# Kernel optimization log

Measured on AMD Instinct MI355X. Metric: run time of the kernel, lower is better.

The kernel has to match this reference:

```python
import jax, jax.numpy as jnp
import numpy as np

N_ANGLES = 8


def setup_inputs() -> dict:
    key = jax.random.key(0)
    ks = jax.random.split(key, 6)
    N, in_size, out_size, K = 20000, 64, 64, 8
    M = N_ANGLES * N            # block-Laplacian dim = 160000
    E = M * 16                  # avg degree 16 -> 2.56M nnz
    x = jax.random.normal(ks[0], (N, in_size), dtype=jnp.float32)
    ls_vals = jax.random.normal(ks[1], (E,), dtype=jnp.float32) * 0.1
    ls_rows = jax.random.randint(ks[2], (E,), 0, M, dtype=jnp.int32)
    ls_cols = jax.random.randint(ks[3], (E,), 0, M, dtype=jnp.int32)
    weight = jax.random.normal(ks[4], (K, N_ANGLES * in_size, out_size), dtype=jnp.float32) * 0.05
    bias = jnp.zeros((out_size,), dtype=jnp.float32)
    return {"x": x, "ls_vals": ls_vals, "weight": weight, "bias": bias,
            "ls_rows": ls_rows, "ls_cols": ls_cols}


def reference(x, ls_vals, weight, bias, ls_rows, ls_cols):
    N, in_size = x.shape
    K = weight.shape[0]
    M = N_ANGLES * N

    def spmm(T):
        # sparse [M,M] @ dense [M,in] via gather + segment_sum
        return jax.ops.segment_sum(ls_vals[:, None] * T[ls_cols], ls_rows,
                                   num_segments=M)

    def feat(T):
        # [n_angles*N, in] -> [N, n_angles*in] (angle-major per node)
        return T.reshape(N_ANGLES, N, in_size).transpose(1, 0, 2).reshape(N, -1)

    Tx0 = jnp.tile(x, (N_ANGLES, 1))                  # [M, in]
    out = feat(Tx0) @ weight[0]                       # [N, out]
    Tx1 = spmm(Tx0)
    out = out + feat(Tx1) @ weight[1]
    for k in range(2, K):
        Tx2 = 2.0 * spmm(Tx1) - Tx0
        out = out + feat(Tx2) @ weight[k]
        Tx0, Tx1 = Tx1, Tx2
    return out + bias
```

## Files before the change

kernel.cpp:

```cpp
#include <hip/hip_runtime.h>
#include <hip/hip_bf16.h>

#define N_NODES 20000
#define NANG 8
#define CH 64
#define M_ROWS (NANG * N_NODES)
#define E_EDGES (M_ROWS * 16)
#define K_CHEB 8
#define WK_STRIDE (NANG * CH * CH)
#define BROWS 256
#define NB (M_ROWS / BROWS)
#define NCHUNK 320
#define CHUNK (E_EDGES / NCHUNK)
#define SPMM_BLOCKS (M_ROWS / 4)
#define KCAT 3648
#define SK_TOTAL 114
#define BCAP 5120
#define GROWS 32
#define GEMM_BLOCKS (N_NODES / GROWS)

typedef short short8 __attribute__((ext_vector_type(8)));
typedef float f32x4 __attribute__((ext_vector_type(4)));

__device__ __forceinline__ float bf2f(ushort u) {
    return __uint_as_float((unsigned int)u << 16);
}


__global__ __launch_bounds__(256) void count_kernel(const int* __restrict__ rows,
                                                    int* __restrict__ chunk_cnt) {
    __shared__ int h[NB];
    int c = blockIdx.x, tid = threadIdx.x;
    for (int i = tid; i < NB; i += 256) h[i] = 0;
    __syncthreads();
    int base = c * CHUNK;
    for (int i = tid; i < CHUNK; i += 256) atomicAdd(&h[rows[base + i] >> 8], 1);
    __syncthreads();
    for (int i = tid; i < NB; i += 256) chunk_cnt[(size_t)c * NB + i] = h[i];
}

__global__ __launch_bounds__(512) void bscan2_kernel(int* __restrict__ chunk_cnt,
                                                     int* __restrict__ btotal) {
    __shared__ int s[512];
    int b = blockIdx.x, t = threadIdx.x;
    int v = (t < NCHUNK) ? chunk_cnt[(size_t)t * NB + b] : 0;
    s[t] = v;
    __syncthreads();
    for (int off = 1; off < 512; off <<= 1) {
        int u = (t >= off) ? s[t - off] : 0;
        __syncthreads();
        s[t] += u;
        __syncthreads();
    }
    if (t < NCHUNK) chunk_cnt[(size_t)t * NB + b] = s[t] - v;
    if (t == 511) btotal[b] = s[511];
}

__global__ void bscan_kernel(const int* __restrict__ btotal, int* __restrict__ bstart) {
    __shared__ int s[1024];
    int t = threadIdx.x;
    int v = (t < NB) ? btotal[t] : 0;
    s[t] = v;
    __syncthreads();
    for (int off = 1; off < 1024; off <<= 1) {
        int u = (t >= off) ? s[t - off] : 0;
        __syncthreads();
        s[t] += u;
        __syncthreads();
    }
    if (t < NB) bstart[t] = s[t] - v;
    if (t == 1023) bstart[NB] = s[1023];
}

__global__ __launch_bounds__(256) void scatter_kernel(
        const int* __restrict__ rows, const int* __restrict__ cols,
        const float* __restrict__ vals, const int* __restrict__ chunk_cnt,
        const int* __restrict__ bstart, int2* __restrict__ bedges) {
    __shared__ int loff[NB];
    int c = blockIdx.x, tid = threadIdx.x;
    for (int i = tid; i < NB; i += 256)
        loff[i] = chunk_cnt[(size_t)c * NB + i] + bstart[i];
    __syncthreads();
    int base = c * CHUNK;
    for (int i = tid; i < CHUNK; i += 256) {
        int e = base + i;
        int r = rows[e];
        int p = atomicAdd(&loff[r >> 8], 1);
        bedges[p] = make_int2(cols[e] | ((r & 255) << 18), __float_as_int(vals[e]));
    }
}

__global__ __launch_bounds__(256) void bucket_group_kernel(
        const int* __restrict__ bstart, const int2* __restrict__ bin,
        int2* __restrict__ bout, int* __restrict__ row_start) {
    __shared__ int cnt[BROWS];
    __shared__ int pref[BROWS];
    __shared__ int fill[BROWS];
    __shared__ int2 ob[BCAP];
    int b = blockIdx.x, tid = threadIdx.x;
    int s = bstart[b], e = bstart[b + 1];
    int n = e - s;
    cnt[tid] = 0;
    __syncthreads();
    int2 eds[20];
    int ni = 0;
    for (int i = tid; i < n; i += 256, ++ni) {
        int2 ed = bin[s + i];
        if (ni < 20) eds[ni] = ed;
        atomicAdd(&cnt[(ed.x >> 18) & 255], 1);
    }
    __syncthreads();
    int v = cnt[tid];
    pref[tid] = v;
    __syncthreads();
#pragma unroll
    for (int off = 1; off < 256; off <<= 1) {
        int u = (tid >= off) ? pref[tid - off] : 0;
        __syncthreads();
        pref[tid] += u;
        __syncthreads();
    }
    int my_excl = pref[tid] - v;
    __syncthreads();
    pref[tid] = my_excl;
    fill[tid] = my_excl;
    __syncthreads();

    if (n <= BCAP) {
        ni = 0;
        for (int i = tid; i < n; i += 256, ++ni) {
            int2 ed = (ni < 20) ? eds[ni] : bin[s + i];
            int p = atomicAdd(&fill[(ed.x >> 18) & 255], 1);
            ob[p] = make_int2(ed.x & 0x3ffff, ed.y);
        }
        __syncthreads();
        for (int i = tid; i < n; i += 256)
            bout[s + i] = ob[i];
    } else {
        ni = 0;
        for (int i = tid; i < n; i += 256, ++ni) {
            int2 ed = (ni < 20) ? eds[ni] : bin[s + i];
            int p = atomicAdd(&fill[(ed.x >> 18) & 255], 1);
            bout[s + p] = make_int2(ed.x & 0x3ffff, ed.y);
        }
    }
    row_start[b * BROWS + tid] = s + pref[tid];
    if (b == NB - 1 && tid == 0) row_start[M_ROWS] = e;
}


__global__ void xconv_kernel(const float* __restrict__ x, ushort* __restrict__ xb) {
    int i = blockIdx.x * 256 + threadIdx.x;
    __hip_bfloat16 v = __float2bfloat16(x[i]);
    xb[i] = *(ushort*)&v;
}

__global__ void wcat_kernel(const float* __restrict__ W, ushort* __restrict__ Wcat) {
    int idx = blockIdx.x * 256 + threadIdx.x;
    int n   = idx / KCAT;
    int kkc = idx - n * KCAT;
    float v;
    if (kkc < 64) {
        v = 0.f;
#pragma unroll
        for (int a = 0; a < NANG; ++a) v += W[(a * 64 + kkc) * 64 + n];
    } else {
        int k  = ((kkc - 64) >> 9) + 1;
        int kk = (kkc - 64) & 511;
        v = W[(size_t)k * WK_STRIDE + kk * 64 + n];
    }
    __hip_bfloat16 b = __float2bfloat16(v);
    Wcat[idx] = *(ushort*)&b;
}


template <int TIN_TILED, int TSUB_MODE>
__global__ __launch_bounds__(256) void spmm_kernel(
        const int* __restrict__ row_start, const int2* __restrict__ edges,
        const ushort* __restrict__ Tin, const ushort* __restrict__ Tsub,
        ushort* __restrict__ Tout, float alpha, float beta) {
    int r = __builtin_amdgcn_readfirstlane((blockIdx.x * 256 + threadIdx.x) >> 6);
    int lane = threadIdx.x & 63;
    if (r >= M_ROWS) return;
    int s = __builtin_amdgcn_readfirstlane(row_start[r]);
    int e = __builtin_amdgcn_readfirstlane(row_start[r + 1]);
    float acc0 = 0.f, acc1 = 0.f;
    for (int base = s; base < e; base += 16) {
        int idx = min(base + (lane & 15), e - 1);
        int2 ed = edges[idx];
#pragma unroll
        for (int i = 0; i < 16; ++i) {
            int col   = __builtin_amdgcn_readlane(ed.x, i);
            int wbits = __builtin_amdgcn_readlane(ed.y, i);
            if (base + i >= e) wbits = 0;
            unsigned c = (unsigned)col;
            if (TIN_TILED) c %= N_NODES;
            const ushort* rowp = Tin + (size_t)c * CH;
            float t = bf2f(rowp[lane]);
            if (i & 1) acc1 = fmaf(__int_as_float(wbits), t, acc1);
            else       acc0 = fmaf(__int_as_float(wbits), t, acc0);
        }
    }
    float acc = acc0 + acc1;
    size_t oi = (size_t)r * CH + lane;
    float v = alpha * acc;
    if (TSUB_MODE == 1) v += beta * bf2f(Tsub[oi]);
    if (TSUB_MODE == 2) v += beta * bf2f(Tsub[(size_t)((unsigned)r % N_NODES) * CH + lane]);
    __hip_bfloat16 o = __float2bfloat16(v);
    Tout[oi] = *(ushort*)&o;
}


__global__ __launch_bounds__(256) void gemm_cat_kernel(
        const ushort* __restrict__ xb,
        const ushort* __restrict__ Tall,
        const ushort* __restrict__ Wcat,
        const float* __restrict__ bias,
        float* __restrict__ out) {
    __shared__ float red[4][16][64];
    int m0 = blockIdx.x * GROWS;
    int w = threadIdx.x >> 6;
    int l = threadIdx.x & 63;
    int lm = l & 15;
    int lq = l >> 4;
    const short* Xp = (const short*)xb;
    const short* Tp = (const short*)Tall;
    const short* Wp = (const short*)Wcat;

    f32x4 acc[2][4];
#pragma unroll
    for (int rg = 0; rg < 2; ++rg)
#pragma unroll
        for (int t = 0; t < 4; ++t) acc[rg][t] = (f32x4){0.f, 0.f, 0.f, 0.f};

    auto LDA = [&](int sk, int rg) -> short8 {
        int u = sk - 2;
        return *(const short8*)(Tp
            + ((size_t)(u >> 4) * M_ROWS + (size_t)((u & 15) >> 1) * N_NODES
               + (m0 + rg * 16 + lm)) * CH
            + (u & 1) * 32 + lq * 8);
    };
    auto LDB = [&](int sk, int t) -> short8 {
        return *(const short8*)(Wp + (size_t)(t * 16 + lm) * KCAT + sk * 32 + lq * 8);
    };

    if (w == 0) {
#pragma unroll
        for (int sk = 0; sk < 2; ++sk) {
            short8 a0 = *(const short8*)(Xp + (size_t)(m0 + lm) * CH + sk * 32 + lq * 8);
            short8 a1 = *(const short8*)(Xp + (size_t)(m0 + 16 + lm) * CH + sk * 32 + lq * 8);
#pragma unroll
            for (int t = 0; t < 4; ++t) {
                short8 bf = LDB(sk, t);
                acc[0][t] = __builtin_amdgcn_mfma_f32_16x16x32_bf16(a0, bf, acc[0][t], 0, 0, 0);
                acc[1][t] = __builtin_amdgcn_mfma_f32_16x16x32_bf16(a1, bf, acc[1][t], 0, 0, 0);
            }
        }
    }

    int tb = 2 + w * 28;
#pragma unroll 2
    for (int i = 0; i < 28; ++i) {
        int sk = tb + i;
        short8 a0 = LDA(sk, 0);
        short8 a1 = LDA(sk, 1);
#pragma unroll
        for (int t = 0; t < 4; ++t) {
            short8 bf = LDB(sk, t);
            acc[0][t] = __builtin_amdgcn_mfma_f32_16x16x32_bf16(a0, bf, acc[0][t], 0, 0, 0);
            acc[1][t] = __builtin_amdgcn_mfma_f32_16x16x32_bf16(a1, bf, acc[1][t], 0, 0, 0);
        }
    }

#pragma unroll
    for (int rg = 0; rg < 2; ++rg) {
        if (rg) __syncthreads();
#pragma unroll
        for (int t = 0; t < 4; ++t)
#pragma unroll
            for (int rI = 0; rI < 4; ++rI) red[w][t * 4 + rI][l] = acc[rg][t][rI];
        __syncthreads();
        int col = w * 16 + lm;
        float b = bias[col];
#pragma unroll
        for (int rI = 0; rI < 4; ++rI) {
            int i2 = w * 4 + rI;
            float sum = red[0][i2][l] + red[1][i2][l] + red[2][i2][l] + red[3][i2][l];
            out[(size_t)(m0 + rg * 16 + lq * 4 + rI) * CH + col] = sum + b;
        }
    }
}


extern "C" void kernel_launch(void* const* d_in, const int* in_sizes, int n_in,
                              void* d_out, int out_size, void* d_ws, size_t ws_size,
                              hipStream_t stream) {
    (void)in_sizes; (void)n_in; (void)out_size; (void)ws_size;
    const float* x       = (const float*)d_in[0];
    const float* ls_vals = (const float*)d_in[1];
    const float* weight  = (const float*)d_in[2];
    const float* bias    = (const float*)d_in[3];
    const int*   ls_rows = (const int*)d_in[4];
    const int*   ls_cols = (const int*)d_in[5];
    float* out = (float*)d_out;

    char* ws = (char*)d_ws;
    size_t off = 0;
    auto alloc = [&](size_t bytes) -> void* {
        void* p = ws + off;
        off += (bytes + 255) & ~(size_t)255;
        return p;
    };
    int*  chunk_cnt = (int*)alloc((size_t)NCHUNK * NB * sizeof(int));
    int*  btotal    = (int*)alloc(NB * sizeof(int));
    int*  bstart    = (int*)alloc((NB + 1) * sizeof(int));
    int*  row_start = (int*)alloc((M_ROWS + 1) * sizeof(int));
    int2* bedges2   = (int2*)alloc((size_t)E_EDGES * sizeof(int2));
    ushort* Wcat = (ushort*)alloc((size_t)64 * KCAT * sizeof(ushort));
    ushort* xb   = (ushort*)alloc((size_t)N_NODES * CH * sizeof(ushort));
    ushort* Tall = (ushort*)alloc((size_t)7 * M_ROWS * CH * sizeof(ushort));
    int2* bedges = (int2*)Tall;

    count_kernel<<<NCHUNK, 256, 0, stream>>>(ls_rows, chunk_cnt);
    bscan2_kernel<<<NB, 512, 0, stream>>>(chunk_cnt, btotal);
    bscan_kernel<<<1, 1024, 0, stream>>>(btotal, bstart);
    scatter_kernel<<<NCHUNK, 256, 0, stream>>>(ls_rows, ls_cols, ls_vals, chunk_cnt,
                                               bstart, bedges);
    bucket_group_kernel<<<NB, 256, 0, stream>>>(bstart, bedges, bedges2, row_start);

    xconv_kernel<<<(N_NODES * CH) / 256, 256, 0, stream>>>(x, xb);
    wcat_kernel<<<(64 * KCAT) / 256, 256, 0, stream>>>(weight, Wcat);

    ushort* T[8];
    for (int k = 1; k < K_CHEB; ++k) T[k] = Tall + (size_t)(k - 1) * M_ROWS * CH;

    spmm_kernel<1, 0><<<SPMM_BLOCKS, 256, 0, stream>>>(
        row_start, bedges2, xb, xb, T[1], 1.f, 0.f);
    spmm_kernel<0, 2><<<SPMM_BLOCKS, 256, 0, stream>>>(
        row_start, bedges2, T[1], xb, T[2], 2.f, -1.f);
    for (int k = 3; k < K_CHEB; ++k) {
        spmm_kernel<0, 1><<<SPMM_BLOCKS, 256, 0, stream>>>(
            row_start, bedges2, T[k - 1], T[k - 2], T[k], 2.f, -1.f);
    }

    gemm_cat_kernel<<<GEMM_BLOCKS, 256, 0, stream>>>(xb, Tall, Wcat, bias, out);
}
```

Before: 663.3 us.

## Process four rows per wave in SpMM with prefetched edge batches

Each wavefront now handles four consecutive CSR rows instead of one. It loads all row bounds and the first edge batch of every row up front, then prefetches the next 16-edge batch while the current one is consumed. It also issues all 16 gathers before the FMAs so more memory loads are in flight. The intent is to hide edge-load and gather latency and to cut per-row launch overhead, at the cost of more registers, fewer waves, and serial processing of rows within a wave.

```diff
diff --git a/kernel.cpp b/kernel.cpp
--- a/kernel.cpp
+++ b/kernel.cpp
@@ -12,7 +12,8 @@
 #define NB (M_ROWS / BROWS)
 #define NCHUNK 320
 #define CHUNK (E_EDGES / NCHUNK)
-#define SPMM_BLOCKS (M_ROWS / 4)
+#define RPW 4
+#define SPMM_BLOCKS (M_ROWS / (4 * RPW))
 #define KCAT 3648
 #define SK_TOTAL 114
 #define BCAP 5120
@@ -179,35 +180,60 @@
         const int* __restrict__ row_start, const int2* __restrict__ edges,
         const ushort* __restrict__ Tin, const ushort* __restrict__ Tsub,
         ushort* __restrict__ Tout, float alpha, float beta) {
-    int r = __builtin_amdgcn_readfirstlane((blockIdx.x * 256 + threadIdx.x) >> 6);
+    int wid = (blockIdx.x * 256 + threadIdx.x) >> 6;
     int lane = threadIdx.x & 63;
-    if (r >= M_ROWS) return;
-    int s = __builtin_amdgcn_readfirstlane(row_start[r]);
-    int e = __builtin_amdgcn_readfirstlane(row_start[r + 1]);
-    float acc0 = 0.f, acc1 = 0.f;
-    for (int base = s; base < e; base += 16) {
-        int idx = min(base + (lane & 15), e - 1);
-        int2 ed = edges[idx];
-#pragma unroll
-        for (int i = 0; i < 16; ++i) {
-            int col   = __builtin_amdgcn_readlane(ed.x, i);
-            int wbits = __builtin_amdgcn_readlane(ed.y, i);
-            if (base + i >= e) wbits = 0;
-            unsigned c = (unsigned)col;
-            if (TIN_TILED) c %= N_NODES;
-            const ushort* rowp = Tin + (size_t)c * CH;
-            float t = bf2f(rowp[lane]);
-            if (i & 1) acc1 = fmaf(__int_as_float(wbits), t, acc1);
-            else       acc0 = fmaf(__int_as_float(wbits), t, acc0);
-        }
-    }
-    float acc = acc0 + acc1;
-    size_t oi = (size_t)r * CH + lane;
-    float v = alpha * acc;
-    if (TSUB_MODE == 1) v += beta * bf2f(Tsub[oi]);
-    if (TSUB_MODE == 2) v += beta * bf2f(Tsub[(size_t)((unsigned)r % N_NODES) * CH + lane]);
-    __hip_bfloat16 o = __float2bfloat16(v);
-    Tout[oi] = *(ushort*)&o;
+    int r0 = wid * RPW;
+    int l16 = lane & 15;
+
+    int sb[RPW + 1];
+#pragma unroll
+    for (int j = 0; j <= RPW; ++j)
+        sb[j] = __builtin_amdgcn_readfirstlane(row_start[r0 + j]);
+
+    int2 ed[RPW];
+#pragma unroll
+    for (int j = 0; j < RPW; ++j) {
+        int idx = min(sb[j] + l16, sb[j + 1] - 1);
+        idx = max(idx, 0);
+        ed[j] = edges[idx];
+    }
+
+#pragma unroll
+    for (int j = 0; j < RPW; ++j) {
+        int s = sb[j], e = sb[j + 1];
+        float acc0 = 0.f, acc1 = 0.f;
+        int2 cur = ed[j];
+        for (int base = s; base < e; base += 16) {
+            int2 nxt = cur;
+            if (base + 16 < e) {
+                int idx = min(base + 16 + l16, e - 1);
+                nxt = edges[idx];
+            }
+            ushort raw[16];
+#pragma unroll
+            for (int i = 0; i < 16; ++i) {
+                unsigned c = (unsigned)__builtin_amdgcn_readlane(cur.x, i);
+                if (TIN_TILED) c %= N_NODES;
+                raw[i] = Tin[(size_t)c * CH + lane];
+            }
+#pragma unroll
+            for (int i = 0; i < 16; ++i) {
+                int wbits = __builtin_amdgcn_readlane(cur.y, i);
+                if (base + i >= e) wbits = 0;
+                float t = bf2f(raw[i]);
+                if (i & 1) acc1 = fmaf(__int_as_float(wbits), t, acc1);
+                else       acc0 = fmaf(__int_as_float(wbits), t, acc0);
+            }
+            cur = nxt;
+        }
+        int r = r0 + j;
+        float v = alpha * (acc0 + acc1);
+        size_t oi = (size_t)r * CH + lane;
+        if (TSUB_MODE == 1) v += beta * bf2f(Tsub[oi]);
+        if (TSUB_MODE == 2) v += beta * bf2f(Tsub[(size_t)((unsigned)r % N_NODES) * CH + lane]);
+        __hip_bfloat16 o = __float2bfloat16(v);
+        Tout[oi] = *(ushort*)&o;
+    }
 }
 
 
```

Result: faster. 615.8 us (-7.2%).
